# Kernel tuning notes

Measured on AMD Instinct MI355X. Metric: run time of the kernel, lower is better.

## Reference

```python
import jax, jax.numpy as jnp
import numpy as np
from jax import lax

RES = 14
DIM = 384
KEY_DIM = 32
NUM_HEADS = 12
ATTN_RATIO = 4
NH_KD = KEY_DIM * NUM_HEADS            # 384
DH = ATTN_RATIO * KEY_DIM * NUM_HEADS  # 1536
HQKV = DH + 2 * NH_KD                  # 2304
BN_EPS = 1e-5


def _bias_idxs():
    ys, xs = np.meshgrid(np.arange(RES), np.arange(RES), indexing='ij')
    ys = ys.reshape(-1); xs = xs.reshape(-1)
    dy = np.abs(ys[:, None] - ys[None, :])
    dx = np.abs(xs[:, None] - xs[None, :])
    return jnp.asarray(dy * RES + dx, dtype=jnp.int32)  # [196,196], 196 unique offsets


def setup_inputs() -> dict:
    key = jax.random.key(0)
    ks = jax.random.split(key, 16)
    B = 128
    x = jax.random.normal(ks[0], (B, DIM, RES, RES), dtype=jnp.float32)
    # qkv: 1x1 conv DIM->HQKV + BN
    qkv_w = jax.random.normal(ks[1], (HQKV, DIM, 1, 1), dtype=jnp.float32) * 0.05
    qkv_g = jax.random.normal(ks[2], (HQKV,), dtype=jnp.float32) * 0.1 + 1.0
    qkv_b = jax.random.normal(ks[3], (HQKV,), dtype=jnp.float32) * 0.1
    qkv_m = jax.random.normal(ks[4], (HQKV,), dtype=jnp.float32) * 0.1
    qkv_v = jax.random.uniform(ks[5], (HQKV,), dtype=jnp.float32) + 0.5
    # dw: depthwise 3x3 conv on q channels + BN
    dw_w = jax.random.normal(ks[6], (NH_KD, 1, 3, 3), dtype=jnp.float32) * 0.2
    dw_g = jax.random.normal(ks[7], (NH_KD,), dtype=jnp.float32) * 0.1 + 1.0
    dw_b = jax.random.normal(ks[8], (NH_KD,), dtype=jnp.float32) * 0.1
    dw_m = jax.random.normal(ks[9], (NH_KD,), dtype=jnp.float32) * 0.1
    dw_v = jax.random.uniform(ks[10], (NH_KD,), dtype=jnp.float32) + 0.5
    # proj: ReLU -> 1x1 conv DH->DIM + BN
    proj_w = jax.random.normal(ks[11], (DIM, DH, 1, 1), dtype=jnp.float32) * 0.05
    proj_g = jax.random.normal(ks[12], (DIM,), dtype=jnp.float32) * 0.1 + 1.0
    proj_b = jax.random.normal(ks[13], (DIM,), dtype=jnp.float32) * 0.1
    proj_m = jax.random.normal(ks[14], (DIM,), dtype=jnp.float32) * 0.1
    proj_v = jax.random.uniform(ks[15], (DIM,), dtype=jnp.float32) + 0.5
    ab = jax.random.normal(jax.random.fold_in(key, 99), (NUM_HEADS, RES * RES), dtype=jnp.float32) * 0.1
    return {
        'x': x,
        'qkv_w': qkv_w, 'qkv_g': qkv_g, 'qkv_b': qkv_b, 'qkv_m': qkv_m, 'qkv_v': qkv_v,
        'dw_w': dw_w, 'dw_g': dw_g, 'dw_b': dw_b, 'dw_m': dw_m, 'dw_v': dw_v,
        'proj_w': proj_w, 'proj_g': proj_g, 'proj_b': proj_b, 'proj_m': proj_m, 'proj_v': proj_v,
        'attn_biases': ab,
        'bias_idxs': _bias_idxs(),
    }


def _bn(x, g, b, m, v):
    scale = g / jnp.sqrt(v + BN_EPS)
    return x * scale[None, :, None, None] + (b - m * scale)[None, :, None, None]


def reference(x, qkv_w, qkv_g, qkv_b, qkv_m, qkv_v,
              dw_w, dw_g, dw_b, dw_m, dw_v,
              proj_w, proj_g, proj_b, proj_m, proj_v,
              attn_biases, bias_idxs):
    B, _, H, W = x.shape
    n = H * W
    scale = KEY_DIM ** -0.5
    # 1x1 conv + BN
    qkv = jnp.einsum('bchw,oc->bohw', x, qkv_w[:, :, 0, 0])
    qkv = _bn(qkv, qkv_g, qkv_b, qkv_m, qkv_v)
    q = qkv[:, :NH_KD]
    k = qkv[:, NH_KD:2 * NH_KD]
    v = qkv[:, 2 * NH_KD:]
    # depthwise 3x3 conv + BN on q
    q = lax.conv_general_dilated(q, dw_w, (1, 1), ((1, 1), (1, 1)),
                                 dimension_numbers=('NCHW', 'OIHW', 'NCHW'),
                                 feature_group_count=NH_KD)
    q = _bn(q, dw_g, dw_b, dw_m, dw_v)
    # heads: [b, h, d, n]
    q = q.reshape(B, NUM_HEADS, KEY_DIM, n)
    k = k.reshape(B, NUM_HEADS, KEY_DIM, n)
    v = v.reshape(B, NUM_HEADS, ATTN_RATIO * KEY_DIM, n)
    bias = attn_biases[:, bias_idxs]  # [h, n, n]
    attn = jnp.einsum('bhdn,bhdm->bhnm', q, k) * scale + bias[None]
    attn = jax.nn.softmax(attn, axis=-1)
    out = jnp.einsum('bhdm,bhnm->bhdn', v, attn).reshape(B, DH, H, W)
    out = jax.nn.relu(out)
    out = jnp.einsum('bchw,oc->bohw', out, proj_w[:, :, 0, 0])
    return _bn(out, proj_g, proj_b, proj_m, proj_v)
```

## Files before the change

### kernel.cpp

```cpp
#include <hip/hip_runtime.h>

typedef __bf16 bf16;
typedef bf16 bf16x8 __attribute__((ext_vector_type(8)));
typedef bf16 bf16x4 __attribute__((ext_vector_type(4)));
typedef short short4v __attribute__((ext_vector_type(4)));
typedef float f32x4 __attribute__((ext_vector_type(4)));

#define NPIX 196
#define CIN 384
#define NHEADS 12
#define MPAD 224
#define VSTRIDE 232
#define OSTRIDE 40
#define TSTRIDE 136

__device__ __forceinline__ float ldf(const void* p, size_t i, int f) {
    return f ? ((const float*)p)[i] : (float)((const bf16*)p)[i];
}

__device__ __forceinline__ void gld16(const void* g, void* lds_wave_base) {
    __builtin_amdgcn_global_load_lds(
        (const __attribute__((address_space(1))) void*)(unsigned long long)g,
        (__attribute__((address_space(3))) void*)(unsigned long long)lds_wave_base,
        16, 0, 0);
}

__device__ __forceinline__ int xcd_swizzle(int orig, int nwg) {
    int q = nwg >> 3, r = nwg & 7;
    int xcd = orig & 7, idx = orig >> 3;
    return (xcd < r ? xcd * (q + 1) : r * (q + 1) + (xcd - r) * q) + idx;
}

__device__ __forceinline__ f32x4 mfma16(bf16x4 a, bf16x4 b, f32x4 c) {
#if __has_builtin(__builtin_amdgcn_mfma_f32_16x16x16bf16_1k)
    return __builtin_amdgcn_mfma_f32_16x16x16bf16_1k(
        __builtin_bit_cast(short4v, a), __builtin_bit_cast(short4v, b), c, 0, 0, 0);
#else
    asm volatile("v_mfma_f32_16x16x16_bf16 %0, %1, %2, %0" : "+v"(c) : "v"(a), "v"(b));
    return c;
#endif
}

__device__ __forceinline__ f32x4 vmax4(f32x4 a, f32x4 b) {
    f32x4 r;
    r[0] = fmaxf(a[0], b[0]);
    r[1] = fmaxf(a[1], b[1]);
    r[2] = fmaxf(a[2], b[2]);
    r[3] = fmaxf(a[3], b[3]);
    return r;
}

__global__ void detect_kernel(const unsigned int* __restrict__ x, int* __restrict__ flag) {
    __shared__ int cnt;
    if (threadIdx.x == 0) cnt = 0;
    __syncthreads();
    int c = 0;
#pragma unroll
    for (int k = 0; k < 8; k++) {
        unsigned int w = x[threadIdx.x * 8 + k];
        unsigned int e = (w >> 7) & 0xFFu;
        if (e > 200u) c++;
    }
    atomicAdd(&cnt, c);
    __syncthreads();
    if (threadIdx.x == 0) *flag = (cnt >= 16) ? 1 : 0;
}

__global__ void convert_kernel(const void* __restrict__ src, bf16* __restrict__ dst, int n,
                               const int* __restrict__ flag) {
    int f = *flag;
    for (int i = blockIdx.x * 256 + threadIdx.x; i < n; i += gridDim.x * 256)
        dst[i] = (bf16)ldf(src, i, f);
}

__global__ void transpose_x_kernel(const void* __restrict__ x, const int* __restrict__ flag,
                                   bf16* __restrict__ xt, int b0) {
    __shared__ bf16 tile[32][33];
    int f = *flag;
    int b = blockIdx.z, gb = b0 + b;
    int c0 = blockIdx.y * 32;
    int hw0 = blockIdx.x * 32;
    int tx = threadIdx.x, ty = threadIdx.y;
    int hw = hw0 + tx, c = c0 + ty;
    if (hw < NPIX) tile[ty][tx] = (bf16)ldf(x, ((size_t)gb * CIN + c) * NPIX + hw, f);
    __syncthreads();
    int hw2 = hw0 + ty, c2 = c0 + tx;
    if (hw2 < NPIX) xt[((size_t)b * NPIX + hw2) * CIN + c2] = tile[tx][ty];
}

template <int K>
__device__ __forceinline__ void gemm_tile32(const bf16* __restrict__ A, const bf16* __restrict__ B,
                                            bf16* smem, f32x4 acc[4][4]) {
    int tid = threadIdx.x;
    int wave = tid >> 6, lane = tid & 63;
    int wm = wave >> 1, wn = wave & 1;
    int row = lane & 15, grp = lane >> 4;
    int sr = lane >> 2;
    int scg = (lane & 3) ^ (sr & 3);
    const int BUF = 128 * 32;
    bf16* As = smem;
    bf16* Bs = smem + 2 * BUF;
    const bf16* Ag = A + (size_t)(wave * 16 + sr) * K + scg * 8;
    const bf16* Bg = B + (size_t)(wave * 16 + sr) * K + scg * 8;
#pragma unroll
    for (int p = 0; p < 2; p++) {
        gld16(Ag + (size_t)(p * 64) * K, As + (p * 256 + wave * 64) * 8);
        gld16(Bg + (size_t)(p * 64) * K, Bs + (p * 256 + wave * 64) * 8);
    }
    int cur = 0;
#pragma unroll 1
    for (int kb = 0; kb < K; kb += 32) {
        if (kb + 32 < K) {
            bf16* Asn = As + (cur ^ 1) * BUF;
            bf16* Bsn = Bs + (cur ^ 1) * BUF;
#pragma unroll
            for (int p = 0; p < 2; p++) {
                gld16(Ag + (size_t)(p * 64) * K + kb + 32, Asn + (p * 256 + wave * 64) * 8);
                gld16(Bg + (size_t)(p * 64) * K + kb + 32, Bsn + (p * 256 + wave * 64) * 8);
            }
            __builtin_amdgcn_sched_barrier(0);
            asm volatile("s_waitcnt vmcnt(4)" ::: "memory");
        } else {
            __builtin_amdgcn_sched_barrier(0);
            asm volatile("s_waitcnt vmcnt(0)" ::: "memory");
        }
        __builtin_amdgcn_s_barrier();
        __builtin_amdgcn_sched_barrier(0);
        const bf16* Asc = As + cur * BUF;
        const bf16* Bsc = Bs + cur * BUF;
        bf16x8 af[4], bfr[4];
#pragma unroll
        for (int t = 0; t < 4; t++) {
            int ra = wm * 64 + t * 16 + row;
            af[t] = *(const bf16x8*)(Asc + ra * 32 + ((grp ^ (ra & 3)) * 8));
            int rb = wn * 64 + t * 16 + row;
            bfr[t] = *(const bf16x8*)(Bsc + rb * 32 + ((grp ^ (rb & 3)) * 8));
        }
#pragma unroll
        for (int mt = 0; mt < 4; mt++)
#pragma unroll
            for (int nt = 0; nt < 4; nt++)
                acc[mt][nt] =
                    __builtin_amdgcn_mfma_f32_16x16x32_bf16(af[mt], bfr[nt], acc[mt][nt], 0, 0, 0);
        __builtin_amdgcn_sched_barrier(0);
        __builtin_amdgcn_s_barrier();
        cur ^= 1;
    }
    __builtin_amdgcn_sched_barrier(0);
}

__global__ __launch_bounds__(256) void gemm_qkv_kernel(
    const bf16* __restrict__ xt, const bf16* __restrict__ w,
    const void* __restrict__ g, const void* __restrict__ bb,
    const void* __restrict__ mm, const void* __restrict__ vv, const int* __restrict__ flag,
    bf16* __restrict__ qb, bf16* __restrict__ kt, bf16* __restrict__ vb) {
    __shared__ bf16 smem[128 * TSTRIDE];
    f32x4 acc[4][4];
#pragma unroll
    for (int i = 0; i < 4; i++)
#pragma unroll
        for (int j = 0; j < 4; j++) acc[i][j] = (f32x4){0.f, 0.f, 0.f, 0.f};
    int nwg = gridDim.x * gridDim.y;
    int l = xcd_swizzle(blockIdx.y * gridDim.x + blockIdx.x, nwg);
    int m0 = (l % gridDim.x) * 128, n0 = (l / gridDim.x) * 128;
    gemm_tile32<CIN>(w + (size_t)m0 * CIN, xt + (size_t)n0 * CIN, smem, acc);
    int f = *flag;
    int tid = threadIdx.x;
    int wave = tid >> 6, lane = tid & 63;
    int wm = wave >> 1, wn = wave & 1, row = lane & 15, grp = lane >> 4;
    if (m0 >= 384 && m0 < 768) {
        bf16* tbuf = smem;
#pragma unroll
        for (int mt = 0; mt < 4; mt++) {
#pragma unroll
            for (int r = 0; r < 4; r++) {
                int ol = wm * 64 + mt * 16 + grp * 4 + r;
                int o = m0 + ol;
                float scv = ldf(g, o, f) * rsqrtf(ldf(vv, o, f) + 1e-5f);
                float sh = ldf(bb, o, f) - ldf(mm, o, f) * scv;
#pragma unroll
                for (int nt = 0; nt < 4; nt++) {
                    int nl = wn * 64 + nt * 16 + row;
                    tbuf[nl * TSTRIDE + ol] = (bf16)(acc[mt][nt][r] * scv + sh);
                }
            }
        }
        __syncthreads();
#pragma unroll
        for (int it = 0; it < 8; it++) {
            int g2 = it * 256 + tid;
            int nl = g2 >> 4, ch = g2 & 15;
            *(bf16x8*)(kt + (size_t)(n0 + nl) * CIN + (m0 - 384) + ch * 8) =
                *(const bf16x8*)(tbuf + nl * TSTRIDE + ch * 8);
        }
    } else {
#pragma unroll
        for (int mt = 0; mt < 4; mt++) {
#pragma unroll
            for (int r = 0; r < 4; r++) {
                int o = m0 + wm * 64 + mt * 16 + grp * 4 + r;
                float scv = ldf(g, o, f) * rsqrtf(ldf(vv, o, f) + 1e-5f);
                float sh = ldf(bb, o, f) - ldf(mm, o, f) * scv;
#pragma unroll
                for (int nt = 0; nt < 4; nt++) {
                    int n = n0 + wn * 64 + nt * 16 + row;
                    int b = n / NPIX, hw = n - b * NPIX;
                    float val = acc[mt][nt][r] * scv + sh;
                    bf16 bv = (bf16)val;
                    if (o < 384) {
                        qb[((size_t)b * 384 + o) * NPIX + hw] = bv;
                    } else {
                        vb[((size_t)b * 1536 + (o - 768)) * MPAD + hw] = bv;
                    }
                }
            }
        }
    }
}

__global__ __launch_bounds__(256) void gemm_proj_kernel(
    const bf16* __restrict__ ot, const bf16* __restrict__ w,
    const void* __restrict__ g, const void* __restrict__ bb,
    const void* __restrict__ mm, const void* __restrict__ vv, const int* __restrict__ flag,
    void* __restrict__ out, int b0) {
    __shared__ bf16 smem[4 * 128 * 32];
    f32x4 acc[4][4];
#pragma unroll
    for (int i = 0; i < 4; i++)
#pragma unroll
        for (int j = 0; j < 4; j++) acc[i][j] = (f32x4){0.f, 0.f, 0.f, 0.f};
    int nwg = gridDim.x * gridDim.y;
    int l = xcd_swizzle(blockIdx.y * gridDim.x + blockIdx.x, nwg);
    int m0 = (l % gridDim.x) * 128, n0 = (l / gridDim.x) * 128;
    gemm_tile32<1536>(w + (size_t)m0 * 1536, ot + (size_t)n0 * 1536, smem, acc);
    int f = *flag;
    int wave = threadIdx.x >> 6, lane = threadIdx.x & 63;
    int wm = wave >> 1, wn = wave & 1, row = lane & 15, grp = lane >> 4;
#pragma unroll
    for (int mt = 0; mt < 4; mt++) {
#pragma unroll
        for (int r = 0; r < 4; r++) {
            int o = m0 + wm * 64 + mt * 16 + grp * 4 + r;
            float scv = ldf(g, o, f) * rsqrtf(ldf(vv, o, f) + 1e-5f);
            float sh = ldf(bb, o, f) - ldf(mm, o, f) * scv;
#pragma unroll
            for (int nt = 0; nt < 4; nt++) {
                int n = n0 + wn * 64 + nt * 16 + row;
                int b = n / NPIX, hw = n - b * NPIX;
                float val = acc[mt][nt][r] * scv + sh;
                size_t oidx = ((size_t)(b0 + b) * 384 + o) * NPIX + hw;
                if (f) ((float*)out)[oidx] = val;
                else ((bf16*)out)[oidx] = (bf16)val;
            }
        }
    }
}

__global__ void dwconv_kernel(const bf16* __restrict__ qb, const bf16* __restrict__ w,
                              const void* __restrict__ g, const void* __restrict__ bb,
                              const void* __restrict__ mm, const void* __restrict__ vv,
                              const int* __restrict__ flag, bf16* __restrict__ qt) {
    __shared__ bf16 tile[32][33];
    int f = *flag;
    int b = blockIdx.z;
    int c0 = blockIdx.y * 32, hw0 = blockIdx.x * 32;
    int tx = threadIdx.x, ty = threadIdx.y;
    int c = c0 + ty, hw = hw0 + tx;
    if (hw < NPIX) {
        int y = hw / 14, x = hw % 14;
        float acc = 0.f;
        const bf16* wp = w + c * 9;
        const bf16* qp = qb + ((size_t)b * 384 + c) * NPIX;
#pragma unroll
        for (int ky = 0; ky < 3; ky++) {
            int yy = y + ky - 1;
            if (yy < 0 || yy >= 14) continue;
#pragma unroll
            for (int kx = 0; kx < 3; kx++) {
                int xx = x + kx - 1;
                if (xx < 0 || xx >= 14) continue;
                acc += (float)qp[yy * 14 + xx] * (float)wp[ky * 3 + kx];
            }
        }
        float sc = ldf(g, c, f) * rsqrtf(ldf(vv, c, f) + 1e-5f);
        float sh = ldf(bb, c, f) - ldf(mm, c, f) * sc;
        tile[ty][tx] = (bf16)(acc * sc + sh);
    }
    __syncthreads();
    int hw2 = hw0 + ty, c2 = c0 + tx;
    if (hw2 < NPIX) qt[((size_t)b * NPIX + hw2) * CIN + c2] = tile[tx][ty];
}

__global__ void bias_gather_kernel(const void* __restrict__ ab, const int* __restrict__ idx,
                                   const int* __restrict__ flag, float* __restrict__ biasf) {
    int f = *flag;
    int t = blockIdx.x * 256 + threadIdx.x;
    if (t >= NHEADS * NPIX * MPAD) return;
    int h = t / (NPIX * MPAD);
    int rem = t - h * (NPIX * MPAD);
    int n = rem / MPAD, m = rem - n * MPAD;
    biasf[t] = (m < NPIX) ? ldf(ab, h * NPIX + idx[n * NPIX + m], f) : -1e30f;
}

__global__ void zero_vpad_kernel(bf16* __restrict__ vb, int rows) {
    int t = blockIdx.x * 256 + threadIdx.x;
    if (t >= rows * 7) return;
    int r = t / 7, c = t - r * 7;
    *(unsigned long long*)(vb + (size_t)r * MPAD + NPIX + c * 4) = 0ull;
}

__global__ __launch_bounds__(256, 2) void attn_kernel(
    const bf16* __restrict__ qt, const bf16* __restrict__ ktp, const bf16* __restrict__ vb,
    const float* __restrict__ biasf, bf16* __restrict__ ot) {
    __shared__ bf16 Vs[128 * VSTRIDE];
    __shared__ bf16 Osh[4][16 * OSTRIDE];
    int nwg = gridDim.x * gridDim.y;
    int l = xcd_swizzle(blockIdx.y * gridDim.x + blockIdx.x, nwg);
    int h = l % NHEADS, b = l / NHEADS;
    int tid = threadIdx.x;
    int wave = tid >> 6, lane = tid & 63;
    int row = lane & 15, grp = lane >> 4;
    const float scale = 0.17677669529663687f;
    const f32x4 zf = {0.f, 0.f, 0.f, 0.f};

    {
        const bf16* vsrc = vb + ((size_t)b * 1536 + h * 128) * MPAD;
#pragma unroll
        for (int it = 0; it < 14; it++) {
            int i = it * 256 + tid;
            int r = i / 28, gch = i - r * 28;
            *(bf16x8*)(Vs + r * VSTRIDE + gch * 8) = *(const bf16x8*)(vsrc + (size_t)i * 8);
        }
    }
    __syncthreads();

    const bf16* vls = Vs + row * VSTRIDE + grp * 4;

    for (int nb = wave; nb < 13; nb += 4) {
        int n0 = nb * 16;
        int n = n0 + row;
        int nc = n > 195 ? 195 : n;

        bf16x8 aq = *(const bf16x8*)(qt + ((size_t)b * NPIX + nc) * CIN + h * 32 + grp * 8);

        f32x4 sacc[14];
#pragma unroll
        for (int mt = 0; mt < 14; mt++) {
            int krow = mt * 16 + row;
            if (krow > 195) krow = 195;
            bf16x8 ak = *(const bf16x8*)(ktp + ((size_t)b * NPIX + krow) * CIN + h * 32 + grp * 8);
            sacc[mt] = __builtin_amdgcn_mfma_f32_16x16x32_bf16(ak, aq, zf, 0, 0, 0);
        }

        const float* bp = biasf + ((size_t)h * NPIX + nc) * MPAD + grp * 4;
        f32x4 mxv = {-3.4e38f, -3.4e38f, -3.4e38f, -3.4e38f};
#pragma unroll
        for (int mt = 0; mt < 14; mt++) {
            f32x4 bv = *(const f32x4*)(bp + mt * 16);
            f32x4 s = sacc[mt] * scale + bv;
            sacc[mt] = s;
            mxv = vmax4(mxv, s);
        }
        float mx = fmaxf(fmaxf(mxv[0], mxv[1]), fmaxf(mxv[2], mxv[3]));
        mx = fmaxf(mx, __shfl_xor(mx, 16));
        mx = fmaxf(mx, __shfl_xor(mx, 32));

        f32x4 sumv = zf;
        bf16x4 pf[14];
#pragma unroll
        for (int mt = 0; mt < 14; mt++) {
            f32x4 e;
#pragma unroll
            for (int r = 0; r < 4; r++) e[r] = __expf(sacc[mt][r] - mx);
            sumv += e;
            bf16x4 pb;
#pragma unroll
            for (int r = 0; r < 4; r++) pb[r] = (bf16)e[r];
            pf[mt] = pb;
        }
        float sum = (sumv[0] + sumv[1]) + (sumv[2] + sumv[3]);
        sum += __shfl_xor(sum, 16);
        sum += __shfl_xor(sum, 32);
        float inv = 1.f / sum;

        f32x4 oacc[8];
#pragma unroll
        for (int dt = 0; dt < 8; dt++) oacc[dt] = zf;
#pragma unroll
        for (int mt = 0; mt < 14; mt++) {
            bf16x4 p = pf[mt];
#pragma unroll
            for (int dt = 0; dt < 8; dt++) {
                bf16x4 v4 = *(const bf16x4*)(vls + dt * 16 * VSTRIDE + mt * 16);
                oacc[dt] = mfma16(v4, p, oacc[dt]);
            }
        }

        bf16* osw = Osh[wave];
        int r2 = lane >> 2, c2 = lane & 3;
        int n2 = n0 + r2;
        bf16* op = ot + ((size_t)b * NPIX + n2) * 1536 + h * 128;
#pragma unroll
        for (int dp = 0; dp < 4; dp++) {
#pragma unroll
            for (int u = 0; u < 2; u++) {
                int dt = dp * 2 + u;
                bf16x4 o4;
#pragma unroll
                for (int r = 0; r < 4; r++) {
                    float v = oacc[dt][r] * inv;
                    o4[r] = (bf16)(v > 0.f ? v : 0.f);
                }
                *(bf16x4*)(osw + row * OSTRIDE + u * 16 + grp * 4) = o4;
            }
            asm volatile("s_waitcnt lgkmcnt(0)" ::: "memory");
            if (n2 < NPIX) {
                bf16x8 ov = *(const bf16x8*)(osw + r2 * OSTRIDE + c2 * 8);
                *(bf16x8*)(op + dp * 32 + c2 * 8) = ov;
            }
            asm volatile("s_waitcnt lgkmcnt(0)" ::: "memory");
        }
    }
}

extern "C" void kernel_launch(void* const* d_in, const int* in_sizes, int n_in,
                              void* d_out, int out_size, void* d_ws, size_t ws_size,
                              hipStream_t stream) {
    const void* x      = d_in[0];
    const void* qkv_w  = d_in[1];
    const void* qkv_g  = d_in[2];
    const void* qkv_b  = d_in[3];
    const void* qkv_m  = d_in[4];
    const void* qkv_v  = d_in[5];
    const void* dw_w   = d_in[6];
    const void* dw_g   = d_in[7];
    const void* dw_b   = d_in[8];
    const void* dw_m   = d_in[9];
    const void* dw_v   = d_in[10];
    const void* proj_w = d_in[11];
    const void* proj_g = d_in[12];
    const void* proj_b = d_in[13];
    const void* proj_m = d_in[14];
    const void* proj_v = d_in[15];
    const void* ab     = d_in[16];
    const int*  idx    = (const int*)d_in[17];

    char* ws = (char*)d_ws;
    size_t off = 0;
    auto alloc = [&](size_t bytes) { void* p = ws + off; off += (bytes + 255) & ~(size_t)255; return p; };

    int*   flag = (int*)alloc(4);
    bf16*  wq   = (bf16*)alloc((size_t)2304 * 384 * 2);
    bf16*  wp   = (bf16*)alloc((size_t)384 * 1536 * 2);
    bf16*  wd   = (bf16*)alloc((size_t)384 * 9 * 2);
    float* biasf= (float*)alloc((size_t)NHEADS * NPIX * MPAD * 4);
    size_t fixed = off;

    const size_t s_xt = (size_t)NPIX * CIN;
    const size_t s_qb = (size_t)384 * NPIX;
    const size_t s_kt = (size_t)NPIX * 384;
    const size_t s_vb = (size_t)1536 * MPAD;
    const size_t s_ot = (size_t)NPIX * 1536;
    const size_t per_image = (s_xt + s_qb + s_kt + s_vb + s_ot) * 2;

    int CB = 128;
    while (CB > 32 && fixed + (size_t)CB * per_image > ws_size) CB >>= 1;

    bf16* xt  = (bf16*)alloc((size_t)CB * s_xt * 2);
    bf16* qb  = (bf16*)alloc((size_t)CB * s_qb * 2);
    bf16* ktp = (bf16*)alloc((size_t)CB * s_kt * 2);
    bf16* vb  = (bf16*)alloc((size_t)CB * s_vb * 2);
    bf16* ot  = (bf16*)alloc((size_t)CB * s_ot * 2);
    bf16* qt  = xt;

    detect_kernel<<<dim3(1), dim3(256), 0, stream>>>((const unsigned int*)x, flag);
    convert_kernel<<<dim3(256), dim3(256), 0, stream>>>(qkv_w, wq, 2304 * 384, flag);
    convert_kernel<<<dim3(256), dim3(256), 0, stream>>>(proj_w, wp, 384 * 1536, flag);
    convert_kernel<<<dim3(4), dim3(256), 0, stream>>>(dw_w, wd, 384 * 9, flag);
    int bg = (NHEADS * NPIX * MPAD + 255) / 256;
    bias_gather_kernel<<<dim3(bg), dim3(256), 0, stream>>>(ab, idx, flag, biasf);
    int vrows = CB * 1536;
    zero_vpad_kernel<<<dim3((vrows * 7 + 255) / 256), dim3(256), 0, stream>>>(vb, vrows);

    dim3 tb(32, 32);
    for (int b0 = 0; b0 < 128; b0 += CB) {
        int cb = (128 - b0 < CB) ? (128 - b0) : CB;
        int ntiles = (cb * NPIX) / 128;
        transpose_x_kernel<<<dim3(7, 12, cb), tb, 0, stream>>>(x, flag, xt, b0);
        gemm_qkv_kernel<<<dim3(18, ntiles), dim3(256), 0, stream>>>(xt, wq, qkv_g, qkv_b, qkv_m,
                                                                    qkv_v, flag, qb, ktp, vb);
        dwconv_kernel<<<dim3(7, 12, cb), tb, 0, stream>>>(qb, wd, dw_g, dw_b, dw_m, dw_v, flag, qt);
        attn_kernel<<<dim3(NHEADS, cb), dim3(256), 0, stream>>>(qt, ktp, vb, biasf, ot);
        gemm_proj_kernel<<<dim3(3, ntiles), dim3(256), 0, stream>>>(ot, wp, proj_g, proj_b, proj_m,
                                                                    proj_v, flag, d_out, b0);
    }
}
```

Baseline: 459.6 us.

## Use three-stage LDS pipeline in GEMMs and merge prep kernels into one launch

The shared GEMM tile routine moves from a double-buffered loop with two barriers per K-step to a triple-buffered loop with one barrier per step. Loads for stage s+2 are issued after the barrier, and the LDS XOR swizzle now keys on row>>1. The separate weight-convert, bias-gather and V-pad-zero kernels are folded into a single flat-indexed prep kernel, which cuts launch count. The cost is more LDS per GEMM block (24K bf16 elements), which may lower occupancy.

```diff
diff --git a/kernel.cpp b/kernel.cpp
--- a/kernel.cpp
+++ b/kernel.cpp
@@ -13,6 +13,11 @@
 #define VSTRIDE 232
 #define OSTRIDE 40
 #define TSTRIDE 136
+
+#define N_WQ (2304 * 384)
+#define N_WP (384 * 1536)
+#define N_WD (384 * 9)
+#define N_BI (NHEADS * NPIX * MPAD)
 
 __device__ __forceinline__ float ldf(const void* p, size_t i, int f) {
     return f ? ((const float*)p)[i] : (float)((const bf16*)p)[i];
@@ -66,11 +71,31 @@
     if (threadIdx.x == 0) *flag = (cnt >= 16) ? 1 : 0;
 }
 
-__global__ void convert_kernel(const void* __restrict__ src, bf16* __restrict__ dst, int n,
-                               const int* __restrict__ flag) {
+__global__ void prep_kernel(const void* __restrict__ qkv_w, const void* __restrict__ proj_w,
+                            const void* __restrict__ dw_w, const void* __restrict__ ab,
+                            const int* __restrict__ idx, const int* __restrict__ flag,
+                            bf16* __restrict__ wq, bf16* __restrict__ wp, bf16* __restrict__ wd,
+                            float* __restrict__ biasf, bf16* __restrict__ vb, int nvpad) {
     int f = *flag;
-    for (int i = blockIdx.x * 256 + threadIdx.x; i < n; i += gridDim.x * 256)
-        dst[i] = (bf16)ldf(src, i, f);
+    long t = (long)blockIdx.x * 256 + threadIdx.x;
+    if (t < N_WQ) { wq[t] = (bf16)ldf(qkv_w, t, f); return; }
+    t -= N_WQ;
+    if (t < N_WP) { wp[t] = (bf16)ldf(proj_w, t, f); return; }
+    t -= N_WP;
+    if (t < N_WD) { wd[t] = (bf16)ldf(dw_w, t, f); return; }
+    t -= N_WD;
+    if (t < N_BI) {
+        int h = (int)(t / (NPIX * MPAD));
+        int rem = (int)(t - (long)h * (NPIX * MPAD));
+        int n = rem / MPAD, m = rem - n * MPAD;
+        biasf[t] = (m < NPIX) ? ldf(ab, h * NPIX + idx[n * NPIX + m], f) : -1e30f;
+        return;
+    }
+    t -= N_BI;
+    if (t < nvpad) {
+        long r = t / 7, c = t - r * 7;
+        *(unsigned long long*)(vb + r * MPAD + NPIX + c * 4) = 0ull;
+    }
 }
 
 __global__ void transpose_x_kernel(const void* __restrict__ x, const int* __restrict__ flag,
@@ -89,52 +114,56 @@
 }
 
 template <int K>
-__device__ __forceinline__ void gemm_tile32(const bf16* __restrict__ A, const bf16* __restrict__ B,
-                                            bf16* smem, f32x4 acc[4][4]) {
+__device__ __forceinline__ void gemm_tile3(const bf16* __restrict__ A, const bf16* __restrict__ B,
+                                           bf16* smem, f32x4 acc[4][4]) {
+    constexpr int NS = K / 32;
+    const int BUF = 128 * 32;
     int tid = threadIdx.x;
     int wave = tid >> 6, lane = tid & 63;
     int wm = wave >> 1, wn = wave & 1;
     int row = lane & 15, grp = lane >> 4;
     int sr = lane >> 2;
-    int scg = (lane & 3) ^ (sr & 3);
-    const int BUF = 128 * 32;
+    int scg = (lane & 3) ^ ((sr >> 1) & 3);
     bf16* As = smem;
-    bf16* Bs = smem + 2 * BUF;
+    bf16* Bs = smem + 3 * BUF;
     const bf16* Ag = A + (size_t)(wave * 16 + sr) * K + scg * 8;
     const bf16* Bg = B + (size_t)(wave * 16 + sr) * K + scg * 8;
-#pragma unroll
-    for (int p = 0; p < 2; p++) {
-        gld16(Ag + (size_t)(p * 64) * K, As + (p * 256 + wave * 64) * 8);
-        gld16(Bg + (size_t)(p * 64) * K, Bs + (p * 256 + wave * 64) * 8);
-    }
-    int cur = 0;
+    int dbase = (wave * 64) * 8;
+    int rs = (grp ^ ((row >> 1) & 3)) * 8;
+
+#define STAGE3(s, bi)                                                            \
+    {                                                                            \
+        bf16* Ad = As + (bi) * BUF;                                              \
+        bf16* Bd = Bs + (bi) * BUF;                                              \
+        _Pragma("unroll") for (int p = 0; p < 2; p++) {                          \
+            gld16(Ag + (size_t)(p * 64) * K + (s) * 32, Ad + p * 2048 + dbase);  \
+            gld16(Bg + (size_t)(p * 64) * K + (s) * 32, Bd + p * 2048 + dbase);  \
+        }                                                                        \
+    }
+
+    STAGE3(0, 0);
+    STAGE3(1, 1);
+    int cb = 0, nb = 2;
 #pragma unroll 1
-    for (int kb = 0; kb < K; kb += 32) {
-        if (kb + 32 < K) {
-            bf16* Asn = As + (cur ^ 1) * BUF;
-            bf16* Bsn = Bs + (cur ^ 1) * BUF;
-#pragma unroll
-            for (int p = 0; p < 2; p++) {
-                gld16(Ag + (size_t)(p * 64) * K + kb + 32, Asn + (p * 256 + wave * 64) * 8);
-                gld16(Bg + (size_t)(p * 64) * K + kb + 32, Bsn + (p * 256 + wave * 64) * 8);
-            }
-            __builtin_amdgcn_sched_barrier(0);
+    for (int s = 0; s < NS; s++) {
+        __builtin_amdgcn_sched_barrier(0);
+        if (s < NS - 1) {
             asm volatile("s_waitcnt vmcnt(4)" ::: "memory");
         } else {
-            __builtin_amdgcn_sched_barrier(0);
             asm volatile("s_waitcnt vmcnt(0)" ::: "memory");
         }
         __builtin_amdgcn_s_barrier();
         __builtin_amdgcn_sched_barrier(0);
-        const bf16* Asc = As + cur * BUF;
-        const bf16* Bsc = Bs + cur * BUF;
+        if (s + 2 < NS) {
+            STAGE3(s + 2, nb);
+        }
+        const bf16* Asc = As + cb * BUF;
+        const bf16* Bsc = Bs + cb * BUF;
         bf16x8 af[4], bfr[4];
 #pragma unroll
         for (int t = 0; t < 4; t++) {
-            int ra = wm * 64 + t * 16 + row;
-            af[t] = *(const bf16x8*)(Asc + ra * 32 + ((grp ^ (ra & 3)) * 8));
-            int rb = wn * 64 + t * 16 + row;
-            bfr[t] = *(const bf16x8*)(Bsc + rb * 32 + ((grp ^ (rb & 3)) * 8));
+            af[t] = *(const bf16x8*)(Asc + (wm * 64 + t * 16 + row) * 32 + rs);
+            bfr[t] = *(const bf16x8*)(Bsc + (wn * 64 + t * 16 + row) * 32 + rs);
         }
 #pragma unroll
         for (int mt = 0; mt < 4; mt++)
@@ -142,11 +171,12 @@
             for (int nt = 0; nt < 4; nt++)
                 acc[mt][nt] =
                     __builtin_amdgcn_mfma_f32_16x16x32_bf16(af[mt], bfr[nt], acc[mt][nt], 0, 0, 0);
-        __builtin_amdgcn_sched_barrier(0);
-        __builtin_amdgcn_s_barrier();
-        cur ^= 1;
-    }
+        cb = (cb == 2) ? 0 : cb + 1;
+        nb = (nb == 2) ? 0 : nb + 1;
+    }
+#undef STAGE3
     __builtin_amdgcn_sched_barrier(0);
+    __builtin_amdgcn_s_barrier();
 }
 
 __global__ __launch_bounds__(256) void gemm_qkv_kernel(
@@ -154,7 +184,7 @@
     const void* __restrict__ g, const void* __restrict__ bb,
     const void* __restrict__ mm, const void* __restrict__ vv, const int* __restrict__ flag,
     bf16* __restrict__ qb, bf16* __restrict__ kt, bf16* __restrict__ vb) {
-    __shared__ bf16 smem[128 * TSTRIDE];
+    __shared__ bf16 smem[6 * 128 * 32];
     f32x4 acc[4][4];
 #pragma unroll
     for (int i = 0; i < 4; i++)
@@ -163,7 +193,7 @@
     int nwg = gridDim.x * gridDim.y;
     int l = xcd_swizzle(blockIdx.y * gridDim.x + blockIdx.x, nwg);
     int m0 = (l % gridDim.x) * 128, n0 = (l / gridDim.x) * 128;
-    gemm_tile32<CIN>(w + (size_t)m0 * CIN, xt + (size_t)n0 * CIN, smem, acc);
+    gemm_tile3<CIN>(w + (size_t)m0 * CIN, xt + (size_t)n0 * CIN, smem, acc);
     int f = *flag;
     int tid = threadIdx.x;
     int wave = tid >> 6, lane = tid & 63;
@@ -223,7 +253,7 @@
     const void* __restrict__ g, const void* __restrict__ bb,
     const void* __restrict__ mm, const void* __restrict__ vv, const int* __restrict__ flag,
     void* __restrict__ out, int b0) {
-    __shared__ bf16 smem[4 * 128 * 32];
+    __shared__ bf16 smem[6 * 128 * 32];
     f32x4 acc[4][4];
 #pragma unroll
     for (int i = 0; i < 4; i++)
@@ -232,7 +262,7 @@
     int nwg = gridDim.x * gridDim.y;
     int l = xcd_swizzle(blockIdx.y * gridDim.x + blockIdx.x, nwg);
     int m0 = (l % gridDim.x) * 128, n0 = (l / gridDim.x) * 128;
-    gemm_tile32<1536>(w + (size_t)m0 * 1536, ot + (size_t)n0 * 1536, smem, acc);
+    gemm_tile3<1536>(w + (size_t)m0 * 1536, ot + (size_t)n0 * 1536, smem, acc);
     int f = *flag;
     int wave = threadIdx.x >> 6, lane = threadIdx.x & 63;
     int wm = wave >> 1, wn = wave & 1, row = lane & 15, grp = lane >> 4;
@@ -289,24 +319,6 @@
     __syncthreads();
     int hw2 = hw0 + ty, c2 = c0 + tx;
     if (hw2 < NPIX) qt[((size_t)b * NPIX + hw2) * CIN + c2] = tile[tx][ty];
-}
-
-__global__ void bias_gather_kernel(const void* __restrict__ ab, const int* __restrict__ idx,
-                                   const int* __restrict__ flag, float* __restrict__ biasf) {
-    int f = *flag;
-    int t = blockIdx.x * 256 + threadIdx.x;
-    if (t >= NHEADS * NPIX * MPAD) return;
-    int h = t / (NPIX * MPAD);
-    int rem = t - h * (NPIX * MPAD);
-    int n = rem / MPAD, m = rem - n * MPAD;
-    biasf[t] = (m < NPIX) ? ldf(ab, h * NPIX + idx[n * NPIX + m], f) : -1e30f;
-}
-
-__global__ void zero_vpad_kernel(bf16* __restrict__ vb, int rows) {
-    int t = blockIdx.x * 256 + threadIdx.x;
-    if (t >= rows * 7) return;
-    int r = t / 7, c = t - r * 7;
-    *(unsigned long long*)(vb + (size_t)r * MPAD + NPIX + c * 4) = 0ull;
 }
 
 __global__ __launch_bounds__(256, 2) void attn_kernel(
@@ -450,10 +462,10 @@
     auto alloc = [&](size_t bytes) { void* p = ws + off; off += (bytes + 255) & ~(size_t)255; return p; };
 
     int*   flag = (int*)alloc(4);
-    bf16*  wq   = (bf16*)alloc((size_t)2304 * 384 * 2);
-    bf16*  wp   = (bf16*)alloc((size_t)384 * 1536 * 2);
-    bf16*  wd   = (bf16*)alloc((size_t)384 * 9 * 2);
-    float* biasf= (float*)alloc((size_t)NHEADS * NPIX * MPAD * 4);
+    bf16*  wq   = (bf16*)alloc((size_t)N_WQ * 2);
+    bf16*  wp   = (bf16*)alloc((size_t)N_WP * 2);
+    bf16*  wd   = (bf16*)alloc((size_t)N_WD * 2);
+    float* biasf= (float*)alloc((size_t)N_BI * 4);
     size_t fixed = off;
 
     const size_t s_xt = (size_t)NPIX * CIN;
@@ -474,13 +486,11 @@
     bf16* qt  = xt;
 
     detect_kernel<<<dim3(1), dim3(256), 0, stream>>>((const unsigned int*)x, flag);
-    convert_kernel<<<dim3(256), dim3(256), 0, stream>>>(qkv_w, wq, 2304 * 384, flag);
-    convert_kernel<<<dim3(256), dim3(256), 0, stream>>>(proj_w, wp, 384 * 1536, flag);
-    convert_kernel<<<dim3(4), dim3(256), 0, stream>>>(dw_w, wd, 384 * 9, flag);
-    int bg = (NHEADS * NPIX * MPAD + 255) / 256;
-    bias_gather_kernel<<<dim3(bg), dim3(256), 0, stream>>>(ab, idx, flag, biasf);
-    int vrows = CB * 1536;
-    zero_vpad_kernel<<<dim3((vrows * 7 + 255) / 256), dim3(256), 0, stream>>>(vb, vrows);
+    int nvpad = CB * 1536 * 7;
+    long prep_total = (long)N_WQ + N_WP + N_WD + N_BI + nvpad;
+    int prep_blocks = (int)((prep_total + 255) / 256);
+    prep_kernel<<<dim3(prep_blocks), dim3(256), 0, stream>>>(qkv_w, proj_w, dw_w, ab, idx, flag,
+                                                             wq, wp, wd, biasf, vb, nvpad);
 
     dim3 tb(32, 32);
     for (int b0 = 0; b0 < 128; b0 += CB) {
```

Result: faster. 433.9 us (-5.6%).
